# Performance work log

Hardware: AMD Instinct MI355X
Metric: run time of the kernel (lower is better)

## Reference

```python
import jax, jax.numpy as jnp
import numpy as np
import math

E = 1024
H = 16
D = E // H  # head_dim = 64
B, T = 2, 2048


def setup_inputs() -> dict:
    key = jax.random.key(0)
    ks = jax.random.split(key, 10)
    s_in = 1.0 / math.sqrt(E)
    s_hd = 1.0 / math.sqrt(D)
    return {
        "hidden_states": jax.random.normal(ks[0], (B, T, E), dtype=jnp.float32),
        # stacked per-head Linear weights (torch Linear: y = x @ W.T + b)
        "Wq": jax.random.uniform(ks[1], (H, E, D), jnp.float32, -s_in, s_in),
        "bq": jax.random.uniform(ks[2], (H, D), jnp.float32, -s_in, s_in),
        "Wk": jax.random.uniform(ks[3], (H, E, D), jnp.float32, -s_in, s_in),
        "bk": jax.random.uniform(ks[4], (H, D), jnp.float32, -s_in, s_in),
        "Wv": jax.random.uniform(ks[5], (H, E, D), jnp.float32, -s_in, s_in),
        "bv": jax.random.uniform(ks[6], (H, D), jnp.float32, -s_in, s_in),
        "Wo": jax.random.uniform(ks[7], (H, D, E), jnp.float32, -s_hd, s_hd),
        "bo": jax.random.uniform(ks[8], (H, E), jnp.float32, -s_hd, s_hd),
        "gate": jnp.ones((H,), dtype=jnp.float32),
    }


def reference(hidden_states, Wq, bq, Wk, bk, Wv, bv, Wo, bo, gate):
    # Batched per-head projections: [B,T,E] x [H,E,D] -> [B,H,T,D]
    Q = jnp.einsum("bte,hed->bhtd", hidden_states, Wq) + bq[None, :, None, :]
    K = jnp.einsum("bte,hed->bhtd", hidden_states, Wk) + bk[None, :, None, :]
    V = jnp.einsum("bte,hed->bhtd", hidden_states, Wv) + bv[None, :, None, :]
    scale = 1.0 / math.sqrt(D)
    scores = jnp.einsum("bhtd,bhsd->bhts", Q, K) * scale  # [B,H,T,T]
    weights = jax.nn.softmax(scores, axis=-1)
    attn = jnp.einsum("bhts,bhsd->bhtd", weights, V)  # [B,H,T,D]
    # Per-head output proj (bias included before gating), gated, summed over heads
    proj = jnp.einsum("bhtd,hde->bhte", attn, Wo) + bo[None, :, None, :]
    out = jnp.sum(proj * gate[None, :, None, None], axis=1)  # [B,T,E]
    return out
```

## Files before the change

kernel.cpp:

```cpp
#include <hip/hip_runtime.h>
#include <math.h>

#define E_DIM 1024
#define H_DIM 16
#define D_DIM 64
#define B_DIM 2
#define T_DIM 2048
#define M_TOT (B_DIM * T_DIM)

typedef __bf16 bf16_t;
typedef bf16_t bf16x2 __attribute__((ext_vector_type(2)));
typedef bf16_t bf16x4 __attribute__((ext_vector_type(4)));
typedef bf16_t bf16x8 __attribute__((ext_vector_type(8)));
typedef float f32x4 __attribute__((ext_vector_type(4)));
typedef float f32x16 __attribute__((ext_vector_type(16)));
typedef unsigned int uint4v __attribute__((ext_vector_type(4)));

#define LOG2E_DIV8 0.18033688011112042f

__device__ __forceinline__ float fast_exp2(float x) {
#if __has_builtin(__builtin_amdgcn_exp2f)
    return __builtin_amdgcn_exp2f(x);
#else
    return __expf(x * 0.6931471805599453f);
#endif
}

__device__ __forceinline__ unsigned pack_bf16x2(float a, float b) {
    bf16x2 t = {(bf16_t)a, (bf16_t)b};
    return __builtin_bit_cast(unsigned, t);
}

__device__ __forceinline__ void swap32(unsigned& a, unsigned& b, int hi) {
    unsigned as = (unsigned)__shfl_xor((int)a, 32);
    unsigned bs = (unsigned)__shfl_xor((int)b, 32);
    unsigned na = hi ? bs : a;
    unsigned nb = hi ? b : as;
    a = na; b = nb;
}

__device__ __forceinline__ void load_lds16(const void* g, void* l) {
    __builtin_amdgcn_global_load_lds(
        (const __attribute__((address_space(1))) unsigned int*)g,
        (__attribute__((address_space(3))) unsigned int*)l, 16, 0, 0);
}

__global__ __launch_bounds__(256) void prep_kernel(
    const float* __restrict__ x,
    const float* __restrict__ Wq, const float* __restrict__ Wk,
    const float* __restrict__ Wv, const float* __restrict__ Wo,
    const float* __restrict__ bo, const float* __restrict__ gate,
    bf16_t* __restrict__ Xb, bf16_t* __restrict__ Wcat,
    bf16_t* __restrict__ Wgt, float* __restrict__ bsum) {
    __shared__ float Tt[64][65];
    const int b = blockIdx.x;
    const int tid = threadIdx.x;

    if (b < 2048) {
        size_t i = ((size_t)b * 256 + tid) * 8;
        float4 a0 = *reinterpret_cast<const float4*>(x + i);
        float4 a1 = *reinterpret_cast<const float4*>(x + i + 4);
        bf16x8 o;
        o[0] = (bf16_t)a0.x; o[1] = (bf16_t)a0.y; o[2] = (bf16_t)a0.z; o[3] = (bf16_t)a0.w;
        o[4] = (bf16_t)a1.x; o[5] = (bf16_t)a1.y; o[6] = (bf16_t)a1.z; o[7] = (bf16_t)a1.w;
        *reinterpret_cast<bf16x8*>(Xb + i) = o;
    } else if (b < 2816) {
        const int idx = b - 2048;
        const int z = idx >> 8;
        const int rem = idx & 255;
        const int h = rem >> 4, et = rem & 15;
        const float* W = z == 0 ? Wq : (z == 1 ? Wk : Wv);
        const int r = tid >> 2, c4 = (tid & 3) * 16;
        const float* src = W + (size_t)h * 65536 + (size_t)(et * 64 + r) * 64 + c4;
        #pragma unroll
        for (int k = 0; k < 16; k += 4) {
            float4 v = *reinterpret_cast<const float4*>(src + k);
            Tt[r][c4 + k + 0] = v.x; Tt[r][c4 + k + 1] = v.y;
            Tt[r][c4 + k + 2] = v.z; Tt[r][c4 + k + 3] = v.w;
        }
        __syncthreads();
        bf16x8 o0, o1;
        #pragma unroll
        for (int k = 0; k < 8; ++k) o0[k] = (bf16_t)Tt[c4 + k][r];
        #pragma unroll
        for (int k = 0; k < 8; ++k) o1[k] = (bf16_t)Tt[c4 + 8 + k][r];
        bf16_t* dst = Wcat + ((size_t)(z * 16 + h) * 64 + r) * 1024 + et * 64 + c4;
        *reinterpret_cast<bf16x8*>(dst) = o0;
        *reinterpret_cast<bf16x8*>(dst + 8) = o1;
    } else if (b < 3072) {
        const int idx = b - 2816;
        const int h = idx >> 4, et = idx & 15;
        const float g = gate[h];
        const int r = tid >> 2, c4 = (tid & 3) * 16;
        const float* src = Wo + (size_t)h * 65536 + (size_t)r * 1024 + et * 64 + c4;
        #pragma unroll
        for (int k = 0; k < 16; k += 4) {
            float4 v = *reinterpret_cast<const float4*>(src + k);
            Tt[r][c4 + k + 0] = v.x * g; Tt[r][c4 + k + 1] = v.y * g;
            Tt[r][c4 + k + 2] = v.z * g; Tt[r][c4 + k + 3] = v.w * g;
        }
        __syncthreads();
        bf16x8 o0, o1;
        #pragma unroll
        for (int k = 0; k < 8; ++k) o0[k] = (bf16_t)Tt[c4 + k][r];
        #pragma unroll
        for (int k = 0; k < 8; ++k) o1[k] = (bf16_t)Tt[c4 + 8 + k][r];
        bf16_t* dst = Wgt + (size_t)(et * 64 + r) * 1024 + h * 64 + c4;
        *reinterpret_cast<bf16x8*>(dst) = o0;
        *reinterpret_cast<bf16x8*>(dst + 8) = o1;
    } else {
        const int e = (b - 3072) * 256 + tid;
        float s = 0.f;
        #pragma unroll
        for (int h = 0; h < H_DIM; ++h) s += gate[h] * bo[h * E_DIM + e];
        bsum[e] = s;
    }
}

__global__ __launch_bounds__(256) void qkv_gemm_kernel(
    const bf16_t* __restrict__ Xb, const bf16_t* __restrict__ Wcat,
    const float* __restrict__ bqp, const float* __restrict__ bkp,
    const float* __restrict__ bvp,
    bf16_t* __restrict__ Qw, bf16_t* __restrict__ Kw, bf16_t* __restrict__ Vtw) {
    const int p = blockIdx.x;
    const int l = (p & 7) * 96 + (p >> 3);
    const int mx = l & 31, ny = l >> 5;
    const int m0 = mx * 128, n0 = ny * 128;
    const int z = n0 >> 10;

    __shared__ bf16_t As[128][32];
    __shared__ bf16_t Bs[128][32];

    const int tid = threadIdx.x;
    const int lane = tid & 63, wid = tid >> 6;
    const int wr = wid >> 1, wc = wid & 1;
    const int lr = lane & 15, lg = lane >> 4;
    const int srow = lane >> 2, scol = (lane & 3) * 8;

    const int b_idx = m0 >> 11;
    const int t00 = m0 & (T_DIM - 1);

    #define QKV_STAGE(k0)                                                          \
        _Pragma("unroll")                                                          \
        for (int j = 0; j < 2; ++j) {                                              \
            load_lds16(Xb + (size_t)(m0 + wid * 32 + j * 16 + srow) * E_DIM + (k0) + scol, \
                       (char*)&As[0][0] + wid * 2048 + j * 1024);                  \
            load_lds16(Wcat + (size_t)(n0 + wid * 32 + j * 16 + srow) * E_DIM + (k0) + scol, \
                       (char*)&Bs[0][0] + wid * 2048 + j * 1024);                  \
        }
    #define QKV_FRAGS                                                              \
        bf16x8 a[4], bb[4];                                                        \
        _Pragma("unroll")                                                          \
        for (int i = 0; i < 4; ++i)                                                \
            a[i] = *reinterpret_cast<const bf16x8*>(&As[wr * 64 + i * 16 + lr][lg * 8]); \
        _Pragma("unroll")                                                          \
        for (int j = 0; j < 4; ++j)                                                \
            bb[j] = *reinterpret_cast<const bf16x8*>(&Bs[wc * 64 + j * 16 + lr][lg * 8]);

    if (z < 2) {
        f32x4 acc[4][4] = {};
        for (int k0 = 0; k0 < E_DIM; k0 += 32) {
            QKV_STAGE(k0);
            __syncthreads();
            QKV_FRAGS;
            __builtin_amdgcn_s_setprio(1);
            #pragma unroll
            for (int j = 0; j < 4; ++j)
                #pragma unroll
                for (int i = 0; i < 4; ++i)
                    acc[j][i] = __builtin_amdgcn_mfma_f32_16x16x32_bf16(bb[j], a[i], acc[j][i], 0, 0, 0);
            __builtin_amdgcn_s_setprio(0);
            __syncthreads();
        }
        const float scale = (z == 0) ? LOG2E_DIV8 : 1.0f;
        const float* bias = (z == 0) ? bqp : bkp;
        bf16_t* Obase = (z == 0) ? Qw : Kw;
        #pragma unroll
        for (int j = 0; j < 4; ++j) {
            const int n = n0 + wc * 64 + j * 16 + lg * 4;
            const int h = (n >> 6) & 15;
            const int dbase = n & 63;
            const float4 bv4 = *reinterpret_cast<const float4*>(&bias[n & 1023]);
            bf16_t* O = Obase + (size_t)(b_idx * H_DIM + h) * T_DIM * 64;
            #pragma unroll
            for (int i = 0; i < 4; ++i) {
                const int t = t00 + wr * 64 + i * 16 + lr;
                bf16x4 t4;
                #pragma unroll
                for (int r = 0; r < 4; ++r)
                    t4[r] = (bf16_t)((acc[j][i][r] + (&bv4.x)[r]) * scale);
                *reinterpret_cast<bf16x4*>(&O[(size_t)t * 64 + dbase]) = t4;
            }
        }
    } else {
        f32x4 acc[4][4] = {};
        for (int k0 = 0; k0 < E_DIM; k0 += 32) {
            QKV_STAGE(k0);
            __syncthreads();
            QKV_FRAGS;
            __builtin_amdgcn_s_setprio(1);
            #pragma unroll
            for (int i = 0; i < 4; ++i)
                #pragma unroll
                for (int j = 0; j < 4; ++j)
                    acc[i][j] = __builtin_amdgcn_mfma_f32_16x16x32_bf16(a[i], bb[j], acc[i][j], 0, 0, 0);
            __builtin_amdgcn_s_setprio(0);
            __syncthreads();
        }
        #pragma unroll
        for (int j = 0; j < 4; ++j) {
            const int n = n0 + wc * 64 + j * 16 + lr;
            const int h = (n >> 6) & 15;
            const int d = n & 63;
            const float bval = bvp[n & 1023];
            bf16_t* O = Vtw + (size_t)(b_idx * H_DIM + h) * 64 * T_DIM + (size_t)d * T_DIM;
            #pragma unroll
            for (int i = 0; i < 4; ++i) {
                const int t = t00 + wr * 64 + i * 16 + lg * 4;
                bf16x4 t4;
                #pragma unroll
                for (int r = 0; r < 4; ++r) t4[r] = (bf16_t)(acc[i][j][r] + bval);
                *reinterpret_cast<bf16x4*>(&O[t]) = t4;
            }
        }
    }
    #undef QKV_STAGE
    #undef QKV_FRAGS
}

__global__ __launch_bounds__(256, 2) void attn_mfma_kernel(
    const bf16_t* __restrict__ Q, const bf16_t* __restrict__ K,
    const bf16_t* __restrict__ Vt, bf16_t* __restrict__ Aw) {
    const int p = blockIdx.x;
    const int l = (p & 7) * 64 + (p >> 3);
    const int qx = l & 15, bh = l >> 4;
    const int b_idx = bh >> 4, h = bh & 15;
    const int q0 = qx * 128;
    const size_t base = (size_t)bh * T_DIM * 64;

    __shared__ bf16_t Ks[2][128][72];
    __shared__ bf16_t Vs[2][64][136];

    const int tid = threadIdx.x;
    const int lane = tid & 63;
    const int w = tid >> 6;
    const int lq = lane & 31;
    const int hi = lane >> 5;

    const int qrow = q0 + w * 32 + lq;
    bf16x8 qb[4];
    #pragma unroll
    for (int kc = 0; kc < 4; ++kc)
        qb[kc] = *reinterpret_cast<const bf16x8*>(
            Q + base + (size_t)qrow * 64 + kc * 16 + hi * 8);

    const int kr = tid >> 1, kc0 = (tid & 1) * 32;
    const int vr = tid >> 2, vc0 = (tid & 3) * 32;

    bf16x8 kreg[4], vreg[4];
    #define ATT_LOAD(s0)                                                           \
        {   const bf16_t* ksrc = K + base + (size_t)((s0) + kr) * 64 + kc0;        \
            const bf16_t* vsrc = Vt + base + (size_t)vr * T_DIM + (s0) + vc0;      \
            _Pragma("unroll")                                                      \
            for (int j = 0; j < 4; ++j) {                                          \
                kreg[j] = *reinterpret_cast<const bf16x8*>(ksrc + j * 8);          \
                vreg[j] = *reinterpret_cast<const bf16x8*>(vsrc + j * 8);          \
            } }
    #define ATT_WRITE(buf)                                                         \
        {   _Pragma("unroll")                                                      \
            for (int j = 0; j < 4; ++j) {                                          \
                *reinterpret_cast<bf16x8*>(&Ks[buf][kr][kc0 + j * 8]) = kreg[j];   \
                *reinterpret_cast<bf16x8*>(&Vs[buf][vr][vc0 + j * 8]) = vreg[j];   \
            } }

    ATT_LOAD(0);
    ATT_WRITE(0);
    __syncthreads();

    float mreg = -INFINITY, lrow = 0.f;
    f32x16 o[2] = {};
    int cur = 0;

    for (int it = 0; it < 16; ++it) {
        if (it < 15) ATT_LOAD((it + 1) * 128);

        f32x16 s32[4] = {};
        __builtin_amdgcn_s_setprio(1);
        #pragma unroll
        for (int sb = 0; sb < 4; ++sb)
            #pragma unroll
            for (int kc = 0; kc < 4; ++kc) {
                bf16x8 ka = *reinterpret_cast<const bf16x8*>(
                    &Ks[cur][sb * 32 + lq][kc * 16 + hi * 8]);
                s32[sb] = __builtin_amdgcn_mfma_f32_32x32x16_bf16(ka, qb[kc], s32[sb], 0, 0, 0);
            }
        __builtin_amdgcn_s_setprio(0);

        float pmax = -INFINITY;
        #pragma unroll
        for (int sb = 0; sb < 4; ++sb)
            #pragma unroll
            for (int r = 0; r < 16; r += 4)
                pmax = fmaxf(pmax, fmaxf(fmaxf(s32[sb][r], s32[sb][r + 1]),
                                         fmaxf(s32[sb][r + 2], s32[sb][r + 3])));
        pmax = fmaxf(pmax, __shfl_xor(pmax, 32));

        if (__any(pmax > mreg + 11.5f)) {
            float newm = fmaxf(mreg, pmax);
            float alpha = fast_exp2(mreg - newm);
            mreg = newm;
            lrow *= alpha;
            o[0] *= alpha;
            o[1] *= alpha;
        }

        float rs = 0.f;
        bf16x8 pa[8];
        #pragma unroll
        for (int sb = 0; sb < 4; ++sb) {
            unsigned Wl[4][2];
            #pragma unroll
            for (int grp = 0; grp < 4; ++grp) {
                float p0 = fast_exp2(s32[sb][grp * 4 + 0] - mreg);
                float p1 = fast_exp2(s32[sb][grp * 4 + 1] - mreg);
                float p2 = fast_exp2(s32[sb][grp * 4 + 2] - mreg);
                float p3 = fast_exp2(s32[sb][grp * 4 + 3] - mreg);
                rs += (p0 + p1) + (p2 + p3);
                Wl[grp][0] = pack_bf16x2(p0, p1);
                Wl[grp][1] = pack_bf16x2(p2, p3);
            }
            #pragma unroll
            for (int kl = 0; kl < 2; ++kl) {
                unsigned a0 = Wl[2 * kl][0], b0 = Wl[2 * kl + 1][0];
                unsigned a1 = Wl[2 * kl][1], b1 = Wl[2 * kl + 1][1];
                swap32(a0, b0, hi);
                swap32(a1, b1, hi);
                uint4v tv = {a0, a1, b0, b1};
                pa[sb * 2 + kl] = __builtin_bit_cast(bf16x8, tv);
            }
        }
        rs += __shfl_xor(rs, 32);
        lrow += rs;

        __builtin_amdgcn_s_setprio(1);
        #pragma unroll
        for (int ks = 0; ks < 8; ++ks)
            #pragma unroll
            for (int db = 0; db < 2; ++db) {
                bf16x8 va = *reinterpret_cast<const bf16x8*>(
                    &Vs[cur][db * 32 + lq][ks * 16 + hi * 8]);
                o[db] = __builtin_amdgcn_mfma_f32_32x32x16_bf16(va, pa[ks], o[db], 0, 0, 0);
            }
        __builtin_amdgcn_s_setprio(0);

        if (it < 15) ATT_WRITE(cur ^ 1);
        __syncthreads();
        cur ^= 1;
    }
    #undef ATT_LOAD
    #undef ATT_WRITE

    const float linv = 1.f / lrow;
    const size_t rowbase = ((size_t)b_idx * T_DIM + qrow) * E_DIM + h * 64;
    #pragma unroll
    for (int db = 0; db < 2; ++db)
        #pragma unroll
        for (int grp = 0; grp < 4; ++grp) {
            bf16x4 t4;
            #pragma unroll
            for (int i = 0; i < 4; ++i)
                t4[i] = (bf16_t)(o[db][grp * 4 + i] * linv);
            *reinterpret_cast<bf16x4*>(
                &Aw[rowbase + db * 32 + grp * 8 + hi * 4]) = t4;
        }
}

__global__ __launch_bounds__(256) void out_gemm_kernel(
    const bf16_t* __restrict__ Aw, const bf16_t* __restrict__ Wgt,
    const float* __restrict__ bsum, float* __restrict__ out) {
    const int p = blockIdx.x;
    const int l = (p & 7) * 64 + (p >> 3);
    const int mx = l & 31, ny = l >> 5;
    const int m0 = mx * 128, n0 = ny * 64;

    __shared__ bf16_t As[128][32];
    __shared__ bf16_t Bs[64][32];

    const int tid = threadIdx.x;
    const int lane = tid & 63, wid = tid >> 6;
    const int wr = wid >> 1, wc = wid & 1;
    const int lr = lane & 15, lg = lane >> 4;
    const int srow = lane >> 2, scol = (lane & 3) * 8;

    f32x4 acc[2][4] = {};

    for (int k0 = 0; k0 < E_DIM; k0 += 32) {
        #pragma unroll
        for (int j = 0; j < 2; ++j)
            load_lds16(Aw + (size_t)(m0 + wid * 32 + j * 16 + srow) * E_DIM + k0 + scol,
                       (char*)&As[0][0] + wid * 2048 + j * 1024);
        load_lds16(Wgt + (size_t)(n0 + wid * 16 + srow) * E_DIM + k0 + scol,
                   (char*)&Bs[0][0] + wid * 1024);
        __syncthreads();
        bf16x8 a[4], bb[2];
        #pragma unroll
        for (int i = 0; i < 4; ++i)
            a[i] = *reinterpret_cast<const bf16x8*>(&As[wr * 64 + i * 16 + lr][lg * 8]);
        #pragma unroll
        for (int j = 0; j < 2; ++j)
            bb[j] = *reinterpret_cast<const bf16x8*>(&Bs[wc * 32 + j * 16 + lr][lg * 8]);
        __builtin_amdgcn_s_setprio(1);
        #pragma unroll
        for (int j = 0; j < 2; ++j)
            #pragma unroll
            for (int i = 0; i < 4; ++i)
                acc[j][i] = __builtin_amdgcn_mfma_f32_16x16x32_bf16(bb[j], a[i], acc[j][i], 0, 0, 0);
        __builtin_amdgcn_s_setprio(0);
        __syncthreads();
    }

    #pragma unroll
    for (int j = 0; j < 2; ++j) {
        const int e = n0 + wc * 32 + j * 16 + lg * 4;
        const float4 bs4 = *reinterpret_cast<const float4*>(&bsum[e]);
        #pragma unroll
        for (int i = 0; i < 4; ++i) {
            const int m = m0 + wr * 64 + i * 16 + lr;
            float4 o4;
            o4.x = acc[j][i][0] + bs4.x;
            o4.y = acc[j][i][1] + bs4.y;
            o4.z = acc[j][i][2] + bs4.z;
            o4.w = acc[j][i][3] + bs4.w;
            *reinterpret_cast<float4*>(&out[(size_t)m * E_DIM + e]) = o4;
        }
    }
}

extern "C" void kernel_launch(void* const* d_in, const int* in_sizes, int n_in,
                              void* d_out, int out_size, void* d_ws, size_t ws_size,
                              hipStream_t stream) {
    const float* hs   = (const float*)d_in[0];
    const float* Wq   = (const float*)d_in[1];
    const float* bq   = (const float*)d_in[2];
    const float* Wk   = (const float*)d_in[3];
    const float* bk   = (const float*)d_in[4];
    const float* Wv   = (const float*)d_in[5];
    const float* bv   = (const float*)d_in[6];
    const float* Wo   = (const float*)d_in[7];
    const float* bo   = (const float*)d_in[8];
    const float* gate = (const float*)d_in[9];
    float* out = (float*)d_out;

    const size_t NX = (size_t)M_TOT * E_DIM;
    const size_t NW = (size_t)H_DIM * D_DIM * E_DIM;
    bf16_t* p = (bf16_t*)d_ws;
    bf16_t* Xb   = p; p += NX;
    bf16_t* Wcat = p; p += 3 * NW;
    bf16_t* Wgt  = p; p += NW;
    bf16_t* Qw   = p; p += NX;
    bf16_t* Kw   = p; p += NX;
    bf16_t* Vtw  = p; p += NX;
    bf16_t* Aw   = p; p += NX;
    float*  bsum = (float*)p;

    prep_kernel<<<dim3(3076), 256, 0, stream>>>(hs, Wq, Wk, Wv, Wo, bo, gate,
                                                Xb, Wcat, Wgt, bsum);

    qkv_gemm_kernel<<<dim3(768), 256, 0, stream>>>(Xb, Wcat, bq, bk, bv, Qw, Kw, Vtw);

    attn_mfma_kernel<<<dim3(512), 256, 0, stream>>>(Qw, Kw, Vtw, Aw);

    out_gemm_kernel<<<dim3(512), 256, 0, stream>>>(Aw, Wgt, bsum, out);
}
```

Measured before the change: 198.1 us.

## Software-pipeline QK^T of next tile with softmax/PV of current tile

The attention loop is restructured into a two-stage ping-pong: the QK^T MFMAs for tile t+1 are issued before the softmax and PV work of tile t. Two score register sets alternate, and K/V LDS buffers are refilled after barriers. The goal is to overlap matrix-core work with the exp/pack/shuffle softmax phase. The cross-half swap also moves to the permlane32_swap builtin when the compiler provides it, replacing two shuffles and selects. The cost is doubled score registers, which risks spills or lower occupancy, and two barriers per tile instead of one.

```diff
diff --git a/kernel.cpp b/kernel.cpp
--- a/kernel.cpp
+++ b/kernel.cpp
@@ -15,6 +15,7 @@
 typedef float f32x4 __attribute__((ext_vector_type(4)));
 typedef float f32x16 __attribute__((ext_vector_type(16)));
 typedef unsigned int uint4v __attribute__((ext_vector_type(4)));
+typedef unsigned int uint2v __attribute__((ext_vector_type(2)));
 
 #define LOG2E_DIV8 0.18033688011112042f
 
@@ -32,11 +33,17 @@
 }
 
 __device__ __forceinline__ void swap32(unsigned& a, unsigned& b, int hi) {
+#if __has_builtin(__builtin_amdgcn_permlane32_swap)
+    (void)hi;
+    uint2v r = __builtin_amdgcn_permlane32_swap(a, b, false, false);
+    a = r[0]; b = r[1];
+#else
     unsigned as = (unsigned)__shfl_xor((int)a, 32);
     unsigned bs = (unsigned)__shfl_xor((int)b, 32);
     unsigned na = hi ? bs : a;
     unsigned nb = hi ? b : as;
     a = na; b = nb;
+#endif
 }
 
 __device__ __forceinline__ void load_lds16(const void* g, void* l) {
@@ -273,92 +280,109 @@
                 *reinterpret_cast<bf16x8*>(&Vs[buf][vr][vc0 + j * 8]) = vreg[j];   \
             } }
 
-    ATT_LOAD(0);
-    ATT_WRITE(0);
+    #define QKT(sArr, buf)                                                         \
+        {   _Pragma("unroll")                                                      \
+            for (int sb = 0; sb < 4; ++sb)                                         \
+                _Pragma("unroll")                                                  \
+                for (int e = 0; e < 16; ++e) sArr[sb][e] = 0.f;                    \
+            __builtin_amdgcn_s_setprio(1);                                         \
+            _Pragma("unroll")                                                      \
+            for (int sb = 0; sb < 4; ++sb)                                         \
+                _Pragma("unroll")                                                  \
+                for (int kc = 0; kc < 4; ++kc) {                                   \
+                    bf16x8 ka = *reinterpret_cast<const bf16x8*>(                  \
+                        &Ks[buf][sb * 32 + lq][kc * 16 + hi * 8]);                 \
+                    sArr[sb] = __builtin_amdgcn_mfma_f32_32x32x16_bf16(ka, qb[kc], sArr[sb], 0, 0, 0); \
+                }                                                                  \
+            __builtin_amdgcn_s_setprio(0);                                         \
+        }
+
+    #define SM_PV(sArr, buf)                                                       \
+        {   float pmax = -INFINITY;                                                \
+            _Pragma("unroll")                                                      \
+            for (int sb = 0; sb < 4; ++sb)                                         \
+                _Pragma("unroll")                                                  \
+                for (int r = 0; r < 16; r += 4)                                    \
+                    pmax = fmaxf(pmax, fmaxf(fmaxf(sArr[sb][r], sArr[sb][r + 1]), \
+                                             fmaxf(sArr[sb][r + 2], sArr[sb][r + 3]))); \
+            pmax = fmaxf(pmax, __shfl_xor(pmax, 32));                              \
+            if (__any(pmax > mreg + 11.5f)) {                                      \
+                float newm = fmaxf(mreg, pmax);                                    \
+                float alpha = fast_exp2(mreg - newm);                              \
+                mreg = newm; lrow *= alpha;                                        \
+                o[0] *= alpha; o[1] *= alpha;                                      \
+            }                                                                      \
+            float rs = 0.f;                                                        \
+            bf16x8 pa[8];                                                          \
+            _Pragma("unroll")                                                      \
+            for (int sb = 0; sb < 4; ++sb) {                                       \
+                unsigned Wl[4][2];                                                 \
+                _Pragma("unroll")                                                  \
+                for (int grp = 0; grp < 4; ++grp) {                                \
+                    float p0 = fast_exp2(sArr[sb][grp * 4 + 0] - mreg);            \
+                    float p1 = fast_exp2(sArr[sb][grp * 4 + 1] - mreg);            \
+                    float p2 = fast_exp2(sArr[sb][grp * 4 + 2] - mreg);            \
+                    float p3 = fast_exp2(sArr[sb][grp * 4 + 3] - mreg);            \
+                    rs += (p0 + p1) + (p2 + p3);                                   \
+                    Wl[grp][0] = pack_bf16x2(p0, p1);                              \
+                    Wl[grp][1] = pack_bf16x2(p2, p3);                              \
+                }                                                                  \
+                _Pragma("unroll")                                                  \
+                for (int kl = 0; kl < 2; ++kl) {                                   \
+                    unsigned a0 = Wl[2 * kl][0], b0 = Wl[2 * kl + 1][0];           \
+                    unsigned a1 = Wl[2 * kl][1], b1 = Wl[2 * kl + 1][1];           \
+                    swap32(a0, b0, hi);                                            \
+                    swap32(a1, b1, hi);                                            \
+                    uint4v tv = {a0, a1, b0, b1};                                  \
+                    pa[sb * 2 + kl] = __builtin_bit_cast(bf16x8, tv);              \
+                }                                                                  \
+            }                                                                      \
+            rs += __shfl_xor(rs, 32);                                              \
+            lrow += rs;                                                            \
+            __builtin_amdgcn_s_setprio(1);                                         \
+            _Pragma("unroll")                                                      \
+            for (int ks = 0; ks < 8; ++ks)                                         \
+                _Pragma("unroll")                                                  \
+                for (int db = 0; db < 2; ++db) {                                   \
+                    bf16x8 va = *reinterpret_cast<const bf16x8*>(                  \
+                        &Vs[buf][db * 32 + lq][ks * 16 + hi * 8]);                 \
+                    o[db] = __builtin_amdgcn_mfma_f32_32x32x16_bf16(va, pa[ks], o[db], 0, 0, 0); \
+                }                                                                  \
+            __builtin_amdgcn_s_setprio(0);                                         \
+        }
+
+    ATT_LOAD(0);   ATT_WRITE(0);
+    ATT_LOAD(128); ATT_WRITE(1);
     __syncthreads();
 
     float mreg = -INFINITY, lrow = 0.f;
     f32x16 o[2] = {};
-    int cur = 0;
-
-    for (int it = 0; it < 16; ++it) {
-        if (it < 15) ATT_LOAD((it + 1) * 128);
-
-        f32x16 s32[4] = {};
-        __builtin_amdgcn_s_setprio(1);
-        #pragma unroll
-        for (int sb = 0; sb < 4; ++sb)
-            #pragma unroll
-            for (int kc = 0; kc < 4; ++kc) {
-                bf16x8 ka = *reinterpret_cast<const bf16x8*>(
-                    &Ks[cur][sb * 32 + lq][kc * 16 + hi * 8]);
-                s32[sb] = __builtin_amdgcn_mfma_f32_32x32x16_bf16(ka, qb[kc], s32[sb], 0, 0, 0);
-            }
-        __builtin_amdgcn_s_setprio(0);
-
-        float pmax = -INFINITY;
-        #pragma unroll
-        for (int sb = 0; sb < 4; ++sb)
-            #pragma unroll
-            for (int r = 0; r < 16; r += 4)
-                pmax = fmaxf(pmax, fmaxf(fmaxf(s32[sb][r], s32[sb][r + 1]),
-                                         fmaxf(s32[sb][r + 2], s32[sb][r + 3])));
-        pmax = fmaxf(pmax, __shfl_xor(pmax, 32));
-
-        if (__any(pmax > mreg + 11.5f)) {
-            float newm = fmaxf(mreg, pmax);
-            float alpha = fast_exp2(mreg - newm);
-            mreg = newm;
-            lrow *= alpha;
-            o[0] *= alpha;
-            o[1] *= alpha;
-        }
-
-        float rs = 0.f;
-        bf16x8 pa[8];
-        #pragma unroll
-        for (int sb = 0; sb < 4; ++sb) {
-            unsigned Wl[4][2];
-            #pragma unroll
-            for (int grp = 0; grp < 4; ++grp) {
-                float p0 = fast_exp2(s32[sb][grp * 4 + 0] - mreg);
-                float p1 = fast_exp2(s32[sb][grp * 4 + 1] - mreg);
-                float p2 = fast_exp2(s32[sb][grp * 4 + 2] - mreg);
-                float p3 = fast_exp2(s32[sb][grp * 4 + 3] - mreg);
-                rs += (p0 + p1) + (p2 + p3);
-                Wl[grp][0] = pack_bf16x2(p0, p1);
-                Wl[grp][1] = pack_bf16x2(p2, p3);
-            }
-            #pragma unroll
-            for (int kl = 0; kl < 2; ++kl) {
-                unsigned a0 = Wl[2 * kl][0], b0 = Wl[2 * kl + 1][0];
-                unsigned a1 = Wl[2 * kl][1], b1 = Wl[2 * kl + 1][1];
-                swap32(a0, b0, hi);
-                swap32(a1, b1, hi);
-                uint4v tv = {a0, a1, b0, b1};
-                pa[sb * 2 + kl] = __builtin_bit_cast(bf16x8, tv);
-            }
-        }
-        rs += __shfl_xor(rs, 32);
-        lrow += rs;
-
-        __builtin_amdgcn_s_setprio(1);
-        #pragma unroll
-        for (int ks = 0; ks < 8; ++ks)
-            #pragma unroll
-            for (int db = 0; db < 2; ++db) {
-                bf16x8 va = *reinterpret_cast<const bf16x8*>(
-                    &Vs[cur][db * 32 + lq][ks * 16 + hi * 8]);
-                o[db] = __builtin_amdgcn_mfma_f32_32x32x16_bf16(va, pa[ks], o[db], 0, 0, 0);
-            }
-        __builtin_amdgcn_s_setprio(0);
-
-        if (it < 15) ATT_WRITE(cur ^ 1);
-        __syncthreads();
-        cur ^= 1;
+    f32x16 sA[4], sB[4];
+
+    QKT(sA, 0);
+
+    #pragma unroll 1
+    for (int j = 0; j < 8; ++j) {
+        const int t0 = 2 * j;
+        if (t0 < 14) ATT_LOAD((t0 + 2) * 128);
+        if (t0 < 15) QKT(sB, 1);
+        SM_PV(sA, 0);
+        __syncthreads();
+        if (t0 < 14) ATT_WRITE(0);
+        __syncthreads();
+
+        const int t1 = t0 + 1;
+        if (t1 < 14) ATT_LOAD((t1 + 2) * 128);
+        if (t1 < 15) QKT(sA, 0);
+        SM_PV(sB, 1);
+        __syncthreads();
+        if (t1 < 14) ATT_WRITE(1);
+        __syncthreads();
     }
     #undef ATT_LOAD
     #undef ATT_WRITE
+    #undef QKT
+    #undef SM_PV
 
     const float linv = 1.f / lrow;
     const size_t rowbase = ((size_t)b_idx * T_DIM + qrow) * E_DIM + h * 64;
```

Result: slower. 205.4 us (+3.7%).
